# Optimization experiments

Hardware: AMD Instinct MI355X
Metric: run time of the kernel (lower is better)

The kernel has to match this reference:

```python
import jax, jax.numpy as jnp
import numpy as np
from jax import lax

B, T, C, H, N = 4, 1024, 2048, 32, 64
KVH = 8            # kv heads -> kv_dim = 512, n_rep = 4
GN_EPS = 0.00064   # group_norm eps from Step3


def _l2norm(x):
    # torch F.normalize(p=2, dim=-1) with eps=1e-12
    n = jnp.linalg.norm(x, axis=-1, keepdims=True)
    return x / jnp.maximum(n, 1e-12)


def _rwkv7_scan(r, decay, k, v, aa, bb, state):
    # all inputs (B,T,H,N); state (B,H,N,N) with layout [value, key]
    def step(S, inp):
        r_t, d_t, k_t, v_t, a_t, b_t = inp  # each (B,H,N)
        sa = jnp.einsum('bhik,bhk->bhi', S, a_t)
        S = (S * d_t[:, :, None, :]
             + sa[..., None] * b_t[:, :, None, :]
             + v_t[..., None] * k_t[:, :, None, :])
        y = jnp.einsum('bhik,bhk->bhi', S, r_t)
        return S, y
    xs = tuple(jnp.moveaxis(t, 1, 0) for t in (r, decay, k, v, aa, bb))  # (T,B,H,N)
    state, ys = lax.scan(step, state, xs)
    return jnp.moveaxis(ys, 0, 1), state  # (B,T,H,N), (B,H,N,N)


def _forward(x, v_first, state, R, R_bias, K, K_bias, V, V_bias, O, O_bias,
             w0, w1, w2, a0, a1, a2, v0, v1, v2, k_k, k_a, r_k, ln_w, ln_b):
    # ---- Step1: projections + gates (hybrid_matmul -> plain matmul in fp32 ref) ----
    r = x @ R.T + R_bias                                   # (B,T,C)
    w_raw = -jax.nn.softplus(-(w0 + jnp.tanh(x @ w1) @ w2)) - 0.6
    k = x @ K.T + K_bias                                   # (B,T,512)
    v = x @ V.T + V_bias
    n_rep = C // K.shape[0]
    k = jnp.repeat(k.reshape(B, T, KVH, N), n_rep, axis=2).reshape(B, T, C)
    v = jnp.repeat(v.reshape(B, T, KVH, N), n_rep, axis=2).reshape(B, T, C)
    a = jax.nn.sigmoid(a0 + (x @ a1) @ a2)
    kk = _l2norm((k * k_k).reshape(B, T, H, N)).reshape(B, T, C)
    k = k * (1.0 + (a - 1.0) * k_a)
    # layer_id != 0: cross-layer value blending
    v = v + (v_first - v) * jax.nn.sigmoid(v0 + (x @ v1) @ v2)
    aa = -kk
    bb = kk * a
    # ---- Step2: fused recurrent rwkv7 (fp32 state) ----
    decay = jnp.exp(-jnp.exp(w_raw.astype(jnp.float32)))
    rs = lambda t: t.astype(jnp.float32).reshape(B, T, H, N)
    y, state_out = _rwkv7_scan(rs(r), decay.reshape(B, T, H, N), rs(k), rs(v), rs(aa), rs(bb), state)
    # ---- Step3: group norm over (T, N) per (batch, head) as in the (B,C,T) permute ----
    mean = y.mean(axis=(1, 3), keepdims=True)
    var = ((y - mean) ** 2).mean(axis=(1, 3), keepdims=True)
    yn = (y - mean) * lax.rsqrt(var + GN_EPS)
    xx = (yn * ln_w.reshape(H, N) + ln_b.reshape(H, N)).reshape(B, T, C)
    bonus = ((r.reshape(B, T, H, N) * k.reshape(B, T, H, N) * r_k.reshape(H, N))
             .sum(-1, keepdims=True) * v.reshape(B, T, H, N)).reshape(B, T, C)
    xx = xx + bonus
    out = xx @ O.T + O_bias
    return out


def setup_inputs() -> dict:
    key = jax.random.key(0)
    ks = jax.random.split(key, 25)
    g = lambda i, shape, s: jax.random.normal(ks[i], shape, dtype=jnp.float32) * s
    return {
        'x': g(0, (B, T, C), 1.0),
        'v_first': g(1, (B, T, C), 1.0),
        'state': jnp.zeros((B, H, N, N), dtype=jnp.float32),
        'R': g(2, (C, C), 0.02), 'R_bias': jnp.zeros((C,), jnp.float32),
        'K': g(3, (KVH * N, C), 0.02), 'K_bias': jnp.zeros((KVH * N,), jnp.float32),
        'V': g(4, (KVH * N, C), 0.02), 'V_bias': jnp.zeros((KVH * N,), jnp.float32),
        'O': g(5, (C, C), 0.02), 'O_bias': jnp.zeros((C,), jnp.float32),
        'w0': g(6, (C,), 0.1), 'w1': g(7, (C, 64), 0.05), 'w2': g(8, (64, C), 0.05),
        'a0': g(9, (C,), 0.1), 'a1': g(10, (C, 64), 0.05), 'a2': g(11, (64, C), 0.05),
        'v0': g(12, (C,), 0.1), 'v1': g(13, (C, 32), 0.05), 'v2': g(14, (32, C), 0.05),
        'k_k': 1.0 + g(15, (C,), 0.05),
        'k_a': 1.0 + g(16, (C,), 0.05),
        'r_k': g(17, (C,), 0.1),
        'ln_w': jnp.ones((C,), jnp.float32),
        'ln_b': jnp.zeros((C,), jnp.float32),
    }


def reference(x, v_first, state, R, R_bias, K, K_bias, V, V_bias, O, O_bias,
              w0, w1, w2, a0, a1, a2, v0, v1, v2, k_k, k_a, r_k, ln_w, ln_b):
    return _forward(x, v_first, state, R, R_bias, K, K_bias, V, V_bias, O, O_bias,
                    w0, w1, w2, a0, a1, a2, v0, v1, v2, k_k, k_a, r_k, ln_w, ln_b)
```

## Files before the change

### kernel.cpp

```cpp
#include <hip/hip_runtime.h>
#include <hip/hip_bf16.h>
#include <math.h>

typedef __attribute__((ext_vector_type(8))) short bf16x8;
typedef __attribute__((ext_vector_type(4))) float f32x4;

__device__ __forceinline__ unsigned short f2b(float f) {
  unsigned u = __float_as_uint(f);
  unsigned r = (u + 0x7FFF + ((u >> 16) & 1)) >> 16;
  return (unsigned short)r;
}

__device__ __forceinline__ void async16(const void* g, void* l) {
  __builtin_amdgcn_global_load_lds(
      (const __attribute__((address_space(1))) unsigned int*)(g),
      (__attribute__((address_space(3))) unsigned int*)(l), 16, 0, 0);
}

__device__ __forceinline__ void async4(const void* g, void* l) {
  __builtin_amdgcn_global_load_lds(
      (const __attribute__((address_space(1))) unsigned int*)(g),
      (__attribute__((address_space(3))) unsigned int*)(l), 4, 0, 0);
}

__device__ __forceinline__ float rowsum16(float x) {
  x += __int_as_float(__builtin_amdgcn_update_dpp(0, __float_as_int(x), 0x121, 0xF, 0xF, false));
  x += __int_as_float(__builtin_amdgcn_update_dpp(0, __float_as_int(x), 0x122, 0xF, 0xF, false));
  x += __int_as_float(__builtin_amdgcn_update_dpp(0, __float_as_int(x), 0x124, 0xF, 0xF, false));
  x += __int_as_float(__builtin_amdgcn_update_dpp(0, __float_as_int(x), 0x128, 0xF, 0xF, false));
  return x;
}

__global__ __launch_bounds__(256) void cvt4_kernel(
    const float* __restrict__ x, const float* __restrict__ R,
    const float* __restrict__ K, const float* __restrict__ V,
    unsigned short* __restrict__ xb, unsigned short* __restrict__ RKVb)
{
  const int bid = blockIdx.x;
  const float* s; unsigned short* d; int i;
  if (bid < 8192)       { s = x; d = xb; i = bid * 256 + threadIdx.x; }
  else if (bid < 12288) { s = R; d = RKVb; i = (bid - 8192) * 256 + threadIdx.x; }
  else if (bid < 13312) { s = K; d = RKVb + 2048 * 2048; i = (bid - 12288) * 256 + threadIdx.x; }
  else                  { s = V; d = RKVb + 2560 * 2048; i = (bid - 13312) * 256 + threadIdx.x; }
  float4 v = ((const float4*)s)[i];
  ushort4 o;
  o.x = f2b(v.x); o.y = f2b(v.y); o.z = f2b(v.z); o.w = f2b(v.w);
  ((ushort4*)d)[i] = o;
}

__global__ __launch_bounds__(256) void cvt_bf16(
    const float* __restrict__ s, unsigned short* __restrict__ d, int n4)
{
  int i = blockIdx.x * 256 + threadIdx.x;
  if (i < n4) {
    float4 v = ((const float4*)s)[i];
    ushort4 o;
    o.x = f2b(v.x); o.y = f2b(v.y); o.z = f2b(v.z); o.w = f2b(v.w);
    ((ushort4*)d)[i] = o;
  }
}

__global__ __launch_bounds__(256) void tcvt_kernel(
    const float* __restrict__ in, unsigned short* __restrict__ out,
    int Kd, int Nd, int ors)
{
  __shared__ unsigned short tile[64][65];
  const int tx = threadIdx.x & 63, ty = threadIdx.x >> 6;
  const int n0 = blockIdx.x * 64, k0 = blockIdx.y * 64;
  #pragma unroll
  for (int j = 0; j < 16; ++j) {
    const int k = k0 + j * 4 + ty;
    const int n = n0 + tx;
    unsigned short v = 0;
    if (k < Kd && n < Nd) v = f2b(in[(size_t)k * Nd + n]);
    tile[j * 4 + ty][tx] = v;
  }
  __syncthreads();
  #pragma unroll
  for (int j = 0; j < 16; ++j) {
    const int n = n0 + j * 4 + ty;
    const int k = k0 + tx;
    if (n < Nd && k < Kd) out[(size_t)n * ors + k] = tile[tx][j * 4 + ty];
  }
}

template<int OUTBF16, int ACT>
__global__ __launch_bounds__(256) void gemm_mfma(
    const unsigned short* __restrict__ A, int lda,
    const unsigned short* __restrict__ B, int ldb,
    const float* __restrict__ bias, void* __restrict__ Cv, int ldc,
    int M, int N, int K)
{
  __shared__ __align__(16) unsigned short As[128 * 32];
  __shared__ __align__(16) unsigned short Bs[128 * 32];
  const int tid = threadIdx.x;
  const int w = tid >> 6, lane = tid & 63;
  const int wr = (w >> 1) * 64, wc = (w & 1) * 64;
  const int row0 = blockIdx.y * 128, col0 = blockIdx.x * 128;

  f32x4 acc[4][4];
  #pragma unroll
  for (int i = 0; i < 4; ++i)
    #pragma unroll
    for (int j = 0; j < 4; ++j)
      acc[i][j] = (f32x4){0.f, 0.f, 0.f, 0.f};

  const int srow = w * 32 + (lane >> 2);
  const int scol = (lane & 3) * 8;
  const int brow0 = (col0 + srow < N) ? (col0 + srow) : 0;
  const int brow1 = (col0 + srow + 16 < N) ? (col0 + srow + 16) : 0;
  const unsigned short* gA0 = A + (size_t)(row0 + srow) * lda + scol;
  const unsigned short* gA1 = gA0 + (size_t)16 * lda;
  const unsigned short* gB0 = B + (size_t)brow0 * ldb + scol;
  const unsigned short* gB1 = B + (size_t)brow1 * ldb + scol;
  unsigned short* lA0 = As + w * 1024;
  unsigned short* lA1 = As + w * 1024 + 512;
  unsigned short* lB0 = Bs + w * 1024;
  unsigned short* lB1 = Bs + w * 1024 + 512;

  const int m16 = lane & 15;
  const int q8  = (lane >> 4) * 8;

  for (int k0 = 0; k0 < K; k0 += 32) {
    async16(gA0, lA0);
    async16(gA1, lA1);
    async16(gB0, lB0);
    async16(gB1, lB1);
    gA0 += 32; gA1 += 32; gB0 += 32; gB1 += 32;
    __syncthreads();
    bf16x8 af[4], bfr[4];
    #pragma unroll
    for (int i = 0; i < 4; ++i) {
      af[i]  = *(const bf16x8*)(As + (wr + i * 16 + m16) * 32 + q8);
      bfr[i] = *(const bf16x8*)(Bs + (wc + i * 16 + m16) * 32 + q8);
    }
    #pragma unroll
    for (int i = 0; i < 4; ++i)
      #pragma unroll
      for (int j = 0; j < 4; ++j)
        acc[i][j] = __builtin_amdgcn_mfma_f32_16x16x32_bf16(af[i], bfr[j], acc[i][j], 0, 0, 0);
    __syncthreads();
  }

  #pragma unroll
  for (int j = 0; j < 4; ++j) {
    const int c_ = col0 + wc + j * 16 + (lane & 15);
    if (c_ < N) {
      const float bv = bias ? bias[c_] : 0.f;
      #pragma unroll
      for (int i = 0; i < 4; ++i) {
        const int r_ = row0 + wr + i * 16 + (lane >> 4) * 4;
        #pragma unroll
        for (int t4 = 0; t4 < 4; ++t4) {
          float v = acc[i][j][t4] + bv;
          if (ACT == 2 && c_ < 64) v = tanhf(v);
          if (OUTBF16)
            ((unsigned short*)Cv)[(size_t)(r_ + t4) * ldc + c_] = f2b(v);
          else
            ((float*)Cv)[(size_t)(r_ + t4) * ldc + c_] = v;
        }
      }
    }
  }
}

__global__ __launch_bounds__(256) void gemm_rkv(
    const unsigned short* __restrict__ A, const unsigned short* __restrict__ B,
    const float* __restrict__ Rb_, const float* __restrict__ Kb_,
    const float* __restrict__ Vb_,
    float* __restrict__ Cr, float* __restrict__ Ck, float* __restrict__ Cvv)
{
  __shared__ __align__(16) unsigned short As[128 * 32];
  __shared__ __align__(16) unsigned short Bs[128 * 32];
  const int tid = threadIdx.x;
  const int w = tid >> 6, lane = tid & 63;
  const int wr = (w >> 1) * 64, wc = (w & 1) * 64;
  const int row0 = blockIdx.y * 128, col0 = blockIdx.x * 128;

  float* Cd; int ldc, cbase; const float* bias;
  if (col0 < 2048)      { Cd = Cr;  ldc = 2048; cbase = col0;        bias = Rb_; }
  else if (col0 < 2560) { Cd = Ck;  ldc = 512;  cbase = col0 - 2048; bias = Kb_; }
  else                  { Cd = Cvv; ldc = 512;  cbase = col0 - 2560; bias = Vb_; }

  f32x4 acc[4][4];
  #pragma unroll
  for (int i = 0; i < 4; ++i)
    #pragma unroll
    for (int j = 0; j < 4; ++j)
      acc[i][j] = (f32x4){0.f, 0.f, 0.f, 0.f};

  const int srow = w * 32 + (lane >> 2);
  const int scol = (lane & 3) * 8;
  const unsigned short* gA0 = A + (size_t)(row0 + srow) * 2048 + scol;
  const unsigned short* gA1 = gA0 + (size_t)16 * 2048;
  const unsigned short* gB0 = B + (size_t)(col0 + srow) * 2048 + scol;
  const unsigned short* gB1 = gB0 + (size_t)16 * 2048;
  unsigned short* lA0 = As + w * 1024;
  unsigned short* lA1 = As + w * 1024 + 512;
  unsigned short* lB0 = Bs + w * 1024;
  unsigned short* lB1 = Bs + w * 1024 + 512;

  const int m16 = lane & 15;
  const int q8  = (lane >> 4) * 8;

  for (int k0 = 0; k0 < 2048; k0 += 32) {
    async16(gA0, lA0);
    async16(gA1, lA1);
    async16(gB0, lB0);
    async16(gB1, lB1);
    gA0 += 32; gA1 += 32; gB0 += 32; gB1 += 32;
    __syncthreads();
    bf16x8 af[4], bfr[4];
    #pragma unroll
    for (int i = 0; i < 4; ++i) {
      af[i]  = *(const bf16x8*)(As + (wr + i * 16 + m16) * 32 + q8);
      bfr[i] = *(const bf16x8*)(Bs + (wc + i * 16 + m16) * 32 + q8);
    }
    #pragma unroll
    for (int i = 0; i < 4; ++i)
      #pragma unroll
      for (int j = 0; j < 4; ++j)
        acc[i][j] = __builtin_amdgcn_mfma_f32_16x16x32_bf16(af[i], bfr[j], acc[i][j], 0, 0, 0);
    __syncthreads();
  }

  #pragma unroll
  for (int j = 0; j < 4; ++j) {
    const int c_ = cbase + wc + j * 16 + (lane & 15);
    const float bv = bias[c_];
    #pragma unroll
    for (int i = 0; i < 4; ++i) {
      const int r_ = row0 + wr + i * 16 + (lane >> 4) * 4;
      #pragma unroll
      for (int t4 = 0; t4 < 4; ++t4)
        Cd[(size_t)(r_ + t4) * ldc + c_] = acc[i][j][t4] + bv;
    }
  }
}

__global__ __launch_bounds__(256) void prep_kernel(
    const float* __restrict__ k_buf, const float* __restrict__ v_buf,
    float* wt_decay, const float* __restrict__ at, float* vt_vf,
    const float* __restrict__ v_first,
    const float* __restrict__ w0, const float* __restrict__ a0,
    const float* __restrict__ v0, const float* __restrict__ k_k,
    const float* __restrict__ k_a,
    float* __restrict__ kf, float* __restrict__ aaq, float* __restrict__ bbq)
{
  const int row = blockIdx.x;
  const int tid = threadIdx.x;
  const int c0 = tid << 3;
  const int h = tid >> 3;
  const int kvoff = (h >> 2) << 6;
  const size_t base = (size_t)row * 2048;
  const size_t kvrow = (size_t)row * 512;
  float kr[8], kkr[8];
  float ss = 0.f;
  #pragma unroll
  for (int e = 0; e < 8; ++e) {
    const int c = c0 + e;
    const float kv = k_buf[kvrow + kvoff + (c & 63)];
    kr[e] = kv;
    const float t = kv * k_k[c];
    kkr[e] = t;
    ss = fmaf(t, t, ss);
  }
  ss += __shfl_xor(ss, 1);
  ss += __shfl_xor(ss, 2);
  ss += __shfl_xor(ss, 4);
  const float inv = 1.f / fmaxf(sqrtf(ss), 1e-12f);
  #pragma unroll
  for (int e = 0; e < 8; ++e) {
    const int c = c0 + e;
    const size_t idx = base + c;
    const float kk = kkr[e] * inv;
    const float a = 1.f / (1.f + expf(-(a0[c] + at[idx])));
    const float u = w0[c] + wt_decay[idx];
    const float sig_u = 1.f / (1.f + expf(-u));
    wt_decay[idx] = expf(-0.5488116360940264f * sig_u);
    kf[idx] = kr[e] * fmaf(a - 1.f, k_a[c], 1.f);
    const float vr = v_buf[kvrow + kvoff + (c & 63)];
    const float sv = 1.f / (1.f + expf(-(v0[c] + vt_vf[idx])));
    vt_vf[idx] = vr + (v_first[idx] - vr) * sv;
    aaq[idx] = -kk;
    bbq[idx] = kk * a;
  }
}

#define WB(n) asm volatile("s_waitcnt vmcnt(" #n ")\n\ts_barrier" ::: "memory")
#define BAR2() asm volatile("s_waitcnt lgkmcnt(0)\n\ts_barrier" ::: "memory")

__global__ __launch_bounds__(256) void scan_kernel(
    const float* __restrict__ rB, const float* __restrict__ dB,
    const float* __restrict__ kB, const float* __restrict__ vB,
    const float* __restrict__ aB, const float* __restrict__ bB,
    const float* __restrict__ state, float* __restrict__ y)
{
  __shared__ float lds[11008];
  const int tid = threadIdx.x;
  const int bid = blockIdx.x;
  const int xcd = bid & 7, bj = bid >> 3;
  const int bm = bj & 3, gq = bj >> 2;
  const int bh = (gq << 3) | xcd;
  const int widx = tid >> 6;
  const int lane = tid & 63;
  const int rg = lane >> 4;
  const int colg = lane & 15;
  const int g = (bm << 2) | widx;
  const int row = (g << 2) + rg;
  const int rowb = (widx << 2) | rg;
  const int b = bh >> 5, h = bh & 31;

  float4 S = *(const float4*)(state + (size_t)bh * 4096 + row * 64 + (colg << 2));

  const unsigned cb = (unsigned)((b * 1024) * 2048 + h * 64);
  const unsigned srow16 = (unsigned)((widx << 2) + rg);
  const unsigned gcol = (unsigned)(colg << 2);
  const unsigned ldsseg = (unsigned)(widx << 8);

  #define STAGE(step0, bofs) do {                                            \
    const unsigned go_ = cb + (unsigned)((step0) + srow16) * 2048u;          \
    async16(rB + go_ + gcol, lds + (bofs) + 0 * 1024 + ldsseg);              \
    async16(dB + go_ + gcol, lds + (bofs) + 1 * 1024 + ldsseg);              \
    async16(kB + go_ + gcol, lds + (bofs) + 2 * 1024 + ldsseg);              \
    async16(aB + go_ + gcol, lds + (bofs) + 3 * 1024 + ldsseg);              \
    async16(bB + go_ + gcol, lds + (bofs) + 4 * 1024 + ldsseg);              \
    async4 (vB + go_ + (unsigned)(bm << 4) + (unsigned)colg,                 \
            lds + (bofs) + 5120 + (widx << 6));                              \
  } while (0)

  #define PROCESS(bofs) do {                                                 \
    const int orr_ = (bofs) + 0 * 1024 + (colg << 2);                        \
    const int od_  = (bofs) + 1 * 1024 + (colg << 2);                        \
    const int ok_  = (bofs) + 2 * 1024 + (colg << 2);                        \
    const int oa_  = (bofs) + 3 * 1024 + (colg << 2);                        \
    const int ob_  = (bofs) + 4 * 1024 + (colg << 2);                        \
    const int ov_  = (bofs) + 5120 + rowb;                                   \
    _Pragma("unroll")                                                        \
    for (int s = 0; s < 16; ++s) {                                           \
      const float4 av = *(const float4*)(lds + oa_ + s * 64);                \
      const float4 dv = *(const float4*)(lds + od_ + s * 64);                \
      const float4 bv = *(const float4*)(lds + ob_ + s * 64);                \
      const float4 kv = *(const float4*)(lds + ok_ + s * 64);                \
      const float4 rv = *(const float4*)(lds + orr_ + s * 64);               \
      const float vv = lds[ov_ + (s << 4)];                                  \
      float t0 = fmaf(S.y, av.y, S.x * av.x);                                \
      t0 = fmaf(S.z, av.z, t0);                                              \
      t0 = fmaf(S.w, av.w, t0);                                              \
      const float sa = rowsum16(t0);                                         \
      S.x = fmaf(S.x, dv.x, fmaf(sa, bv.x, vv * kv.x));                      \
      S.y = fmaf(S.y, dv.y, fmaf(sa, bv.y, vv * kv.y));                      \
      S.z = fmaf(S.z, dv.z, fmaf(sa, bv.z, vv * kv.z));                      \
      S.w = fmaf(S.w, dv.w, fmaf(sa, bv.w, vv * kv.w));                      \
      float t1 = fmaf(S.y, rv.y, S.x * rv.x);                                \
      t1 = fmaf(S.z, rv.z, t1);                                              \
      t1 = fmaf(S.w, rv.w, t1);                                              \
      const float yv = rowsum16(t1);                                         \
      if (colg == 0) lds[10752 + (s << 4) + rowb] = yv;                      \
    }                                                                        \
  } while (0)

  #define YSTORE(step0) do {                                                 \
    const float val_ = lds[10752 + tid];                                     \
    y[cb + (unsigned)((step0) + (tid >> 4)) * 2048u +                        \
      (unsigned)(bm << 4) + (unsigned)(tid & 15)] = val_;                    \
  } while (0)

  STAGE(0, 0);
  STAGE(16, 5376);

  WB(6);
  PROCESS(0);
  BAR2();
  YSTORE(0);
  STAGE(32, 0);

  for (int c = 1; c <= 62; ++c) {
    const int bofs = (c & 1) ? 5376 : 0;
    WB(7);
    PROCESS(bofs);
    BAR2();
    YSTORE(c << 4);
    if (c < 62) STAGE((c + 2) << 4, bofs);
  }

  WB(1);
  PROCESS(5376);
  BAR2();
  YSTORE(1008);

  #undef STAGE
  #undef PROCESS
  #undef YSTORE
}

__global__ __launch_bounds__(256) void gsum_kernel(
    const float* __restrict__ y, float* __restrict__ part)
{
  const int blk = blockIdx.x;
  const int bh = blk >> 3, seg = blk & 7;
  const int b = bh >> 5, h = bh & 31;
  const int tid = threadIdx.x;
  const size_t base = ((size_t)(b * 1024 + seg * 128)) * 2048 + h * 64;
  float s = 0.f, ss = 0.f;
  for (int i = tid; i < 8192; i += 256) {
    const int t = i >> 6, n = i & 63;
    const float v = y[base + (size_t)t * 2048 + n];
    s += v;
    ss = fmaf(v, v, ss);
  }
  #pragma unroll
  for (int o = 1; o < 64; o <<= 1) {
    s  += __shfl_xor(s, o);
    ss += __shfl_xor(ss, o);
  }
  __shared__ float red[8];
  const int wid = tid >> 6;
  if ((tid & 63) == 0) { red[wid] = s; red[4 + wid] = ss; }
  __syncthreads();
  if (tid == 0) {
    const float st  = red[0] + red[1] + red[2] + red[3];
    const float sst = red[4] + red[5] + red[6] + red[7];
    ((float2*)part)[blk] = make_float2(st, sst);
  }
}

__global__ __launch_bounds__(256) void gapply_kernel(
    const float* __restrict__ y, const float* __restrict__ rB,
    const float* __restrict__ kf, const float* __restrict__ vf,
    const float* __restrict__ part, const float* __restrict__ r_k,
    const float* __restrict__ ln_w, const float* __restrict__ ln_b,
    unsigned short* __restrict__ xxb)
{
  const int row = blockIdx.x;
  const int b = row >> 10;
  const int tid = threadIdx.x;
  const int h = tid >> 3;
  const int bh = b * 32 + h;
  float s = 0.f, ss = 0.f;
  #pragma unroll
  for (int j = 0; j < 8; ++j) {
    const float2 pr = ((const float2*)part)[(bh << 3) + j];
    s += pr.x; ss += pr.y;
  }
  const float mean = s * (1.f / 65536.f);
  const float rstd = rsqrtf(ss * (1.f / 65536.f) - mean * mean + 0.00064f);
  const int c0 = tid << 3;
  const size_t base = (size_t)row * 2048 + c0;
  float yv[8], vv[8];
  float p = 0.f;
  #pragma unroll
  for (int e = 0; e < 8; ++e) {
    yv[e] = y[base + e];
    vv[e] = vf[base + e];
    p = fmaf(rB[base + e] * kf[base + e], r_k[c0 + e], p);
  }
  p += __shfl_xor(p, 1);
  p += __shfl_xor(p, 2);
  p += __shfl_xor(p, 4);
  #pragma unroll
  for (int e = 0; e < 8; ++e) {
    const float yn = (yv[e] - mean) * rstd;
    xxb[base + e] = f2b(fmaf(yn, ln_w[c0 + e], ln_b[c0 + e]) + p * vv[e]);
  }
}

extern "C" void kernel_launch(void* const* d_in, const int* in_sizes, int n_in,
                              void* d_out, int out_size, void* d_ws, size_t ws_size,
                              hipStream_t stream) {
  const float* x       = (const float*)d_in[0];
  const float* v_first = (const float*)d_in[1];
  const float* state   = (const float*)d_in[2];
  const float* Rw      = (const float*)d_in[3];
  const float* R_bias  = (const float*)d_in[4];
  const float* Kw      = (const float*)d_in[5];
  const float* K_bias  = (const float*)d_in[6];
  const float* Vw      = (const float*)d_in[7];
  const float* V_bias  = (const float*)d_in[8];
  const float* Ow      = (const float*)d_in[9];
  const float* O_bias  = (const float*)d_in[10];
  const float* w0      = (const float*)d_in[11];
  const float* w1      = (const float*)d_in[12];
  const float* w2      = (const float*)d_in[13];
  const float* a0      = (const float*)d_in[14];
  const float* a1      = (const float*)d_in[15];
  const float* a2      = (const float*)d_in[16];
  const float* v0      = (const float*)d_in[17];
  const float* v1      = (const float*)d_in[18];
  const float* v2      = (const float*)d_in[19];
  const float* k_k     = (const float*)d_in[20];
  const float* k_a     = (const float*)d_in[21];
  const float* r_k     = (const float*)d_in[22];
  const float* ln_w    = (const float*)d_in[23];
  const float* ln_b    = (const float*)d_in[24];

  float* ws = (float*)d_ws;
  float* r_buf = ws;
  float* k_buf = r_buf + 8388608;
  float* v_buf = k_buf + 2097152;
  float* wt    = v_buf + 2097152;
  float* at    = wt    + 8388608;
  float* vt    = at    + 8388608;
  float* kf    = vt    + 8388608;
  float* aaq   = kf    + 8388608;
  float* bbq   = aaq   + 8388608;
  float* part  = bbq   + 8388608;
  unsigned short* xb   = (unsigned short*)bbq;
  unsigned short* RKVb = (unsigned short*)kf;
  unsigned short* hcat = (unsigned short*)(kf + 3200000);
  unsigned short* Bcat = (unsigned short*)(kf + 3600000);
  unsigned short* w2t  = (unsigned short*)(kf + 3800000);
  unsigned short* a2t  = (unsigned short*)(kf + 3900000);
  unsigned short* v2t  = (unsigned short*)(kf + 4000000);
  unsigned short* Ob   = (unsigned short*)wt;
  unsigned short* xxb  = (unsigned short*)aaq;

  dim3 blk(256);
  cvt4_kernel<<<14336, blk, 0, stream>>>(x, Rw, Kw, Vw, xb, RKVb);
  tcvt_kernel<<<dim3(1, 32), blk, 0, stream>>>(w1, Bcat,              2048, 64, 2048);
  tcvt_kernel<<<dim3(1, 32), blk, 0, stream>>>(a1, Bcat + 64 * 2048,  2048, 64, 2048);
  tcvt_kernel<<<dim3(1, 32), blk, 0, stream>>>(v1, Bcat + 128 * 2048, 2048, 32, 2048);
  tcvt_kernel<<<dim3(32, 1), blk, 0, stream>>>(w2, w2t, 64, 2048, 64);
  tcvt_kernel<<<dim3(32, 1), blk, 0, stream>>>(a2, a2t, 64, 2048, 64);
  tcvt_kernel<<<dim3(32, 1), blk, 0, stream>>>(v2, v2t, 32, 2048, 32);
  gemm_mfma<1,2><<<dim3(2, 32), blk, 0, stream>>>(xb, 2048, Bcat, 2048, nullptr,
                                                  hcat, 160, 4096, 160, 2048);
  gemm_rkv<<<dim3(24, 32), blk, 0, stream>>>(xb, RKVb, R_bias, K_bias, V_bias,
                                             r_buf, k_buf, v_buf);
  gemm_mfma<0,0><<<dim3(16, 32), blk, 0, stream>>>(hcat, 160, w2t, 64, nullptr,
                                                   wt, 2048, 4096, 2048, 64);
  gemm_mfma<0,0><<<dim3(16, 32), blk, 0, stream>>>(hcat + 64, 160, a2t, 64, nullptr,
                                                   at, 2048, 4096, 2048, 64);
  gemm_mfma<0,0><<<dim3(16, 32), blk, 0, stream>>>(hcat + 128, 160, v2t, 32, nullptr,
                                                   vt, 2048, 4096, 2048, 32);
  prep_kernel<<<4096, blk, 0, stream>>>(k_buf, v_buf, wt, at, vt, v_first,
                                        w0, a0, v0, k_k, k_a, kf, aaq, bbq);
  float* ybuf = at;
  scan_kernel<<<512, blk, 0, stream>>>(r_buf, wt, kf, vt, aaq, bbq, state, ybuf);
  cvt_bf16<<<4096, blk, 0, stream>>>(Ow, Ob, 1048576);
  gsum_kernel<<<1024, blk, 0, stream>>>(ybuf, part);
  gapply_kernel<<<4096, blk, 0, stream>>>(ybuf, r_buf, kf, vt, part, r_k,
                                          ln_w, ln_b, xxb);
  gemm_mfma<0,0><<<dim3(16, 32), blk, 0, stream>>>(xxb, 2048, Ob, 2048, O_bias,
                                                   (float*)d_out, 2048, 4096, 2048, 2048);
}
```

Before: 816.8 us.

## Halve scan blocks with two state rows per thread, fuse group-norm sums

The scan kernel now gives each thread two state rows, so each (batch, head) is split into two blocks instead of four. This halves the grid to 256 blocks and the redundant loading of the r/d/k/a/b streams into LDS. The scan also accumulates the group-norm sum and sum of squares itself, which removes the separate gsum pass over y. The six weight-transpose launches are merged into one kernel. The cost is fewer blocks than CUs, less parallelism and a longer per-thread dependency chain in the serial scan.

Result: no change. 823.2 us (+0.8%).

```diff
diff --git a/kernel.cpp b/kernel.cpp
--- a/kernel.cpp
+++ b/kernel.cpp
@@ -60,13 +60,26 @@
   }
 }
 
-__global__ __launch_bounds__(256) void tcvt_kernel(
-    const float* __restrict__ in, unsigned short* __restrict__ out,
-    int Kd, int Nd, int ors)
-{
+__global__ __launch_bounds__(256) void tcvt_all(
+    const float* __restrict__ w1, const float* __restrict__ a1,
+    const float* __restrict__ v1, const float* __restrict__ w2,
+    const float* __restrict__ a2, const float* __restrict__ v2,
+    unsigned short* __restrict__ Bcat, unsigned short* __restrict__ w2t,
+    unsigned short* __restrict__ a2t, unsigned short* __restrict__ v2t)
+{
+  const int r = blockIdx.x >> 5, i = blockIdx.x & 31;
+  const float* in; unsigned short* out; int Kd, Nd, ors, bx, by;
+  switch (r) {
+    case 0:  in = w1; out = Bcat;             Kd = 2048; Nd = 64;   ors = 2048; bx = 0; by = i; break;
+    case 1:  in = a1; out = Bcat + 64 * 2048; Kd = 2048; Nd = 64;   ors = 2048; bx = 0; by = i; break;
+    case 2:  in = v1; out = Bcat + 128 * 2048; Kd = 2048; Nd = 32;  ors = 2048; bx = 0; by = i; break;
+    case 3:  in = w2; out = w2t;              Kd = 64;   Nd = 2048; ors = 64;   bx = i; by = 0; break;
+    case 4:  in = a2; out = a2t;              Kd = 64;   Nd = 2048; ors = 64;   bx = i; by = 0; break;
+    default: in = v2; out = v2t;              Kd = 32;   Nd = 2048; ors = 32;   bx = i; by = 0; break;
+  }
   __shared__ unsigned short tile[64][65];
   const int tx = threadIdx.x & 63, ty = threadIdx.x >> 6;
-  const int n0 = blockIdx.x * 64, k0 = blockIdx.y * 64;
+  const int n0 = bx * 64, k0 = by * 64;
   #pragma unroll
   for (int j = 0; j < 16; ++j) {
     const int k = k0 + j * 4 + ty;
@@ -287,46 +300,54 @@
   }
 }
 
-#define WB(n) asm volatile("s_waitcnt vmcnt(" #n ")\n\ts_barrier" ::: "memory")
+#define WB(n) asm volatile("s_waitcnt vmcnt(" #n ") lgkmcnt(0)\n\ts_barrier" ::: "memory")
 #define BAR2() asm volatile("s_waitcnt lgkmcnt(0)\n\ts_barrier" ::: "memory")
 
 __global__ __launch_bounds__(256) void scan_kernel(
     const float* __restrict__ rB, const float* __restrict__ dB,
     const float* __restrict__ kB, const float* __restrict__ vB,
     const float* __restrict__ aB, const float* __restrict__ bB,
-    const float* __restrict__ state, float* __restrict__ y)
-{
-  __shared__ float lds[11008];
+    const float* __restrict__ state, float* __restrict__ y,
+    float* __restrict__ part)
+{
+  __shared__ float lds[11776];
   const int tid = threadIdx.x;
   const int bid = blockIdx.x;
-  const int xcd = bid & 7, bj = bid >> 3;
-  const int bm = bj & 3, gq = bj >> 2;
-  const int bh = (gq << 3) | xcd;
+  const int xcd = bid & 7, j = bid >> 3;
+  const int half = j & 1, bhq = j >> 1;
+  const int bh = (bhq << 3) | xcd;
   const int widx = tid >> 6;
   const int lane = tid & 63;
   const int rg = lane >> 4;
   const int colg = lane & 15;
-  const int g = (bm << 2) | widx;
-  const int row = (g << 2) + rg;
-  const int rowb = (widx << 2) | rg;
+  const int r0b = (widx << 3) + (rg << 1);
+  const int r0 = (half << 5) + r0b;
   const int b = bh >> 5, h = bh & 31;
 
-  float4 S = *(const float4*)(state + (size_t)bh * 4096 + row * 64 + (colg << 2));
+  float4 S0 = *(const float4*)(state + (size_t)bh * 4096 + r0 * 64 + (colg << 2));
+  float4 S1 = *(const float4*)(state + (size_t)bh * 4096 + (r0 + 1) * 64 + (colg << 2));
 
   const unsigned cb = (unsigned)((b * 1024) * 2048 + h * 64);
-  const unsigned srow16 = (unsigned)((widx << 2) + rg);
   const unsigned gcol = (unsigned)(colg << 2);
   const unsigned ldsseg = (unsigned)(widx << 8);
+  const unsigned vrow = (unsigned)(half << 5);
+
+  float sacc = 0.f, ssacc = 0.f;
 
   #define STAGE(step0, bofs) do {                                            \
-    const unsigned go_ = cb + (unsigned)((step0) + srow16) * 2048u;          \
+    const unsigned go_ = cb + (unsigned)((step0) + (tid >> 4)) * 2048u;      \
     async16(rB + go_ + gcol, lds + (bofs) + 0 * 1024 + ldsseg);              \
     async16(dB + go_ + gcol, lds + (bofs) + 1 * 1024 + ldsseg);              \
     async16(kB + go_ + gcol, lds + (bofs) + 2 * 1024 + ldsseg);              \
     async16(aB + go_ + gcol, lds + (bofs) + 3 * 1024 + ldsseg);              \
     async16(bB + go_ + gcol, lds + (bofs) + 4 * 1024 + ldsseg);              \
-    async4 (vB + go_ + (unsigned)(bm << 4) + (unsigned)colg,                 \
-            lds + (bofs) + 5120 + (widx << 6));                              \
+    const unsigned gv0_ = cb + (unsigned)((step0) + (tid >> 5)) * 2048u      \
+                          + vrow + (unsigned)(tid & 31);                     \
+    async4(vB + gv0_, lds + (bofs) + 5120 + (widx << 6));                    \
+    const unsigned t2_ = (unsigned)tid + 256u;                               \
+    const unsigned gv1_ = cb + (unsigned)((step0) + (t2_ >> 5)) * 2048u      \
+                          + vrow + (unsigned)(t2_ & 31);                     \
+    async4(vB + gv1_, lds + (bofs) + 5120 + 256 + (widx << 6));              \
   } while (0)
 
   #define PROCESS(bofs) do {                                                 \
@@ -335,7 +356,7 @@
     const int ok_  = (bofs) + 2 * 1024 + (colg << 2);                        \
     const int oa_  = (bofs) + 3 * 1024 + (colg << 2);                        \
     const int ob_  = (bofs) + 4 * 1024 + (colg << 2);                        \
-    const int ov_  = (bofs) + 5120 + rowb;                                   \
+    const int ov_  = (bofs) + 5120 + r0b;                                    \
     _Pragma("unroll")                                                        \
     for (int s = 0; s < 16; ++s) {                                           \
       const float4 av = *(const float4*)(lds + oa_ + s * 64);                \
@@ -343,41 +364,58 @@
       const float4 bv = *(const float4*)(lds + ob_ + s * 64);                \
       const float4 kv = *(const float4*)(lds + ok_ + s * 64);                \
       const float4 rv = *(const float4*)(lds + orr_ + s * 64);               \
-      const float vv = lds[ov_ + (s << 4)];                                  \
-      float t0 = fmaf(S.y, av.y, S.x * av.x);                                \
-      t0 = fmaf(S.z, av.z, t0);                                              \
-      t0 = fmaf(S.w, av.w, t0);                                              \
-      const float sa = rowsum16(t0);                                         \
-      S.x = fmaf(S.x, dv.x, fmaf(sa, bv.x, vv * kv.x));                      \
-      S.y = fmaf(S.y, dv.y, fmaf(sa, bv.y, vv * kv.y));                      \
-      S.z = fmaf(S.z, dv.z, fmaf(sa, bv.z, vv * kv.z));                      \
-      S.w = fmaf(S.w, dv.w, fmaf(sa, bv.w, vv * kv.w));                      \
-      float t1 = fmaf(S.y, rv.y, S.x * rv.x);                                \
-      t1 = fmaf(S.z, rv.z, t1);                                              \
-      t1 = fmaf(S.w, rv.w, t1);                                              \
-      const float yv = rowsum16(t1);                                         \
-      if (colg == 0) lds[10752 + (s << 4) + rowb] = yv;                      \
+      const float2 vv = *(const float2*)(lds + ov_ + (s << 5));              \
+      float t0a = fmaf(S0.y, av.y, S0.x * av.x);                             \
+      t0a = fmaf(S0.z, av.z, t0a);                                           \
+      t0a = fmaf(S0.w, av.w, t0a);                                           \
+      float t0b = fmaf(S1.y, av.y, S1.x * av.x);                             \
+      t0b = fmaf(S1.z, av.z, t0b);                                           \
+      t0b = fmaf(S1.w, av.w, t0b);                                           \
+      const float sa0 = rowsum16(t0a);                                       \
+      const float sa1 = rowsum16(t0b);                                       \
+      S0.x = fmaf(S0.x, dv.x, fmaf(sa0, bv.x, vv.x * kv.x));                 \
+      S0.y = fmaf(S0.y, dv.y, fmaf(sa0, bv.y, vv.x * kv.y));                 \
+      S0.z = fmaf(S0.z, dv.z, fmaf(sa0, bv.z, vv.x * kv.z));                 \
+      S0.w = fmaf(S0.w, dv.w, fmaf(sa0, bv.w, vv.x * kv.w));                 \
+      S1.x = fmaf(S1.x, dv.x, fmaf(sa1, bv.x, vv.y * kv.x));                 \
+      S1.y = fmaf(S1.y, dv.y, fmaf(sa1, bv.y, vv.y * kv.y));                 \
+      S1.z = fmaf(S1.z, dv.z, fmaf(sa1, bv.z, vv.y * kv.z));                 \
+      S1.w = fmaf(S1.w, dv.w, fmaf(sa1, bv.w, vv.y * kv.w));                 \
+      float t1a = fmaf(S0.y, rv.y, S0.x * rv.x);                             \
+      t1a = fmaf(S0.z, rv.z, t1a);                                           \
+      t1a = fmaf(S0.w, rv.w, t1a);                                           \
+      float t1b = fmaf(S1.y, rv.y, S1.x * rv.x);                             \
+      t1b = fmaf(S1.z, rv.z, t1b);                                           \
+      t1b = fmaf(S1.w, rv.w, t1b);                                           \
+      const float y0 = rowsum16(t1a);                                        \
+      const float y1 = rowsum16(t1b);                                        \
+      if (colg == 0) {                                                       \
+        *(float2*)(lds + 11264 + (s << 5) + r0b) = make_float2(y0, y1);      \
+        sacc += y0 + y1;                                                     \
+        ssacc = fmaf(y0, y0, fmaf(y1, y1, ssacc));                           \
+      }                                                                      \
     }                                                                        \
   } while (0)
 
   #define YSTORE(step0) do {                                                 \
-    const float val_ = lds[10752 + tid];                                     \
-    y[cb + (unsigned)((step0) + (tid >> 4)) * 2048u +                        \
-      (unsigned)(bm << 4) + (unsigned)(tid & 15)] = val_;                    \
+    const float2 v_ = *(const float2*)(lds + 11264 + ((tid >> 4) << 5)       \
+                                       + ((tid & 15) << 1));                 \
+    *(float2*)(y + cb + (unsigned)((step0) + (tid >> 4)) * 2048u             \
+               + vrow + (unsigned)((tid & 15) << 1)) = v_;                   \
   } while (0)
 
   STAGE(0, 0);
-  STAGE(16, 5376);
-
-  WB(6);
+  STAGE(16, 5632);
+
+  WB(7);
   PROCESS(0);
   BAR2();
   YSTORE(0);
   STAGE(32, 0);
 
   for (int c = 1; c <= 62; ++c) {
-    const int bofs = (c & 1) ? 5376 : 0;
-    WB(7);
+    const int bofs = (c & 1) ? 5632 : 0;
+    WB(8);
     PROCESS(bofs);
     BAR2();
     YSTORE(c << 4);
@@ -385,44 +423,26 @@
   }
 
   WB(1);
-  PROCESS(5376);
+  PROCESS(5632);
   BAR2();
   YSTORE(1008);
+
+  sacc  += __shfl_xor(sacc, 16);
+  sacc  += __shfl_xor(sacc, 32);
+  ssacc += __shfl_xor(ssacc, 16);
+  ssacc += __shfl_xor(ssacc, 32);
+  __syncthreads();
+  if (lane == 0) { lds[widx] = sacc; lds[4 + widx] = ssacc; }
+  __syncthreads();
+  if (tid == 0) {
+    const float s_  = lds[0] + lds[1] + lds[2] + lds[3];
+    const float ss_ = lds[4] + lds[5] + lds[6] + lds[7];
+    ((float2*)part)[(bh << 1) + half] = make_float2(s_, ss_);
+  }
 
   #undef STAGE
   #undef PROCESS
   #undef YSTORE
-}
-
-__global__ __launch_bounds__(256) void gsum_kernel(
-    const float* __restrict__ y, float* __restrict__ part)
-{
-  const int blk = blockIdx.x;
-  const int bh = blk >> 3, seg = blk & 7;
-  const int b = bh >> 5, h = bh & 31;
-  const int tid = threadIdx.x;
-  const size_t base = ((size_t)(b * 1024 + seg * 128)) * 2048 + h * 64;
-  float s = 0.f, ss = 0.f;
-  for (int i = tid; i < 8192; i += 256) {
-    const int t = i >> 6, n = i & 63;
-    const float v = y[base + (size_t)t * 2048 + n];
-    s += v;
-    ss = fmaf(v, v, ss);
-  }
-  #pragma unroll
-  for (int o = 1; o < 64; o <<= 1) {
-    s  += __shfl_xor(s, o);
-    ss += __shfl_xor(ss, o);
-  }
-  __shared__ float red[8];
-  const int wid = tid >> 6;
-  if ((tid & 63) == 0) { red[wid] = s; red[4 + wid] = ss; }
-  __syncthreads();
-  if (tid == 0) {
-    const float st  = red[0] + red[1] + red[2] + red[3];
-    const float sst = red[4] + red[5] + red[6] + red[7];
-    ((float2*)part)[blk] = make_float2(st, sst);
-  }
 }
 
 __global__ __launch_bounds__(256) void gapply_kernel(
@@ -439,8 +459,8 @@
   const int bh = b * 32 + h;
   float s = 0.f, ss = 0.f;
   #pragma unroll
-  for (int j = 0; j < 8; ++j) {
-    const float2 pr = ((const float2*)part)[(bh << 3) + j];
+  for (int j = 0; j < 2; ++j) {
+    const float2 pr = ((const float2*)part)[(bh << 1) + j];
     s += pr.x; ss += pr.y;
   }
   const float mean = s * (1.f / 65536.f);
@@ -517,12 +537,7 @@
 
   dim3 blk(256);
   cvt4_kernel<<<14336, blk, 0, stream>>>(x, Rw, Kw, Vw, xb, RKVb);
-  tcvt_kernel<<<dim3(1, 32), blk, 0, stream>>>(w1, Bcat,              2048, 64, 2048);
-  tcvt_kernel<<<dim3(1, 32), blk, 0, stream>>>(a1, Bcat + 64 * 2048,  2048, 64, 2048);
-  tcvt_kernel<<<dim3(1, 32), blk, 0, stream>>>(v1, Bcat + 128 * 2048, 2048, 32, 2048);
-  tcvt_kernel<<<dim3(32, 1), blk, 0, stream>>>(w2, w2t, 64, 2048, 64);
-  tcvt_kernel<<<dim3(32, 1), blk, 0, stream>>>(a2, a2t, 64, 2048, 64);
-  tcvt_kernel<<<dim3(32, 1), blk, 0, stream>>>(v2, v2t, 32, 2048, 32);
+  tcvt_all<<<192, blk, 0, stream>>>(w1, a1, v1, w2, a2, v2, Bcat, w2t, a2t, v2t);
   gemm_mfma<1,2><<<dim3(2, 32), blk, 0, stream>>>(xb, 2048, Bcat, 2048, nullptr,
                                                   hcat, 160, 4096, 160, 2048);
   gemm_rkv<<<dim3(24, 32), blk, 0, stream>>>(xb, RKVb, R_bias, K_bias, V_bias,
@@ -536,9 +551,9 @@
   prep_kernel<<<4096, blk, 0, stream>>>(k_buf, v_buf, wt, at, vt, v_first,
                                         w0, a0, v0, k_k, k_a, kf, aaq, bbq);
   float* ybuf = at;
-  scan_kernel<<<512, blk, 0, stream>>>(r_buf, wt, kf, vt, aaq, bbq, state, ybuf);
+  scan_kernel<<<256, blk, 0, stream>>>(r_buf, wt, kf, vt, aaq, bbq, state, ybuf,
+                                       part);
   cvt_bf16<<<4096, blk, 0, stream>>>(Ow, Ob, 1048576);
-  gsum_kernel<<<1024, blk, 0, stream>>>(ybuf, part);
   gapply_kernel<<<4096, blk, 0, stream>>>(ybuf, r_buf, kf, vt, part, r_k,
                                           ln_w, ln_b, xxb);
   gemm_mfma<0,0><<<dim3(16, 32), blk, 0, stream>>>(xxb, 2048, Ob, 2048, O_bias,
```
